# Optimization experiments

Measured on AMD Instinct MI355X. Metric: run time of the kernel, lower is better.

The kernel has to match this reference:

```python
import jax, jax.numpy as jnp
import numpy as np

LOW_THRESH = 0.3
HIGH_THRESH = 0.7
BATCH_SIZE = 256
NUM_POS = BATCH_SIZE // 2   # 128; guaranteed <= total_pos since B2=512 GT boxes are scattered positive
NUM_NEG = BATCH_SIZE - NUM_POS


def _xcycwh_to_x1y1x2y2(b):
    xc, yc, w, h = b[..., 0], b[..., 1], b[..., 2], b[..., 3]
    return jnp.stack([xc - w / 2, yc - h / 2, xc + w / 2, yc + h / 2], axis=-1)


def box_iou(box1, box2):
    # box1: (1, B1, 4), box2: (1, B2, 4) in (xc, yc, w, h) -> iou (1, B1, B2)
    area1 = box1[..., 2] * box1[..., 3]              # (1, B1)
    area2 = box2[..., 2] * box2[..., 3]              # (1, B2)
    c1 = _xcycwh_to_x1y1x2y2(box1)[:, :, None, :]    # (1, B1, 1, 4)
    c2 = _xcycwh_to_x1y1x2y2(box2)[:, None, :, :]    # (1, 1, B2, 4)
    x0 = jnp.maximum(c1[..., 0], c2[..., 0])
    y0 = jnp.maximum(c1[..., 1], c2[..., 1])
    x1 = jnp.minimum(c1[..., 2], c2[..., 2])
    y1 = jnp.minimum(c1[..., 3], c2[..., 3])
    inter = jnp.maximum(x1 - x0, 0.0) * jnp.maximum(y1 - y0, 0.0)  # (1, B1, B2)
    return inter / (area1[:, :, None] + area2[:, None, :] - inter)


def setup_inputs() -> dict:
    key = jax.random.key(0)
    k1, k2, k3, k4 = jax.random.split(key, 4)
    return {
        "input_boxes": jax.random.uniform(k1, (1, 50000, 4), dtype=jnp.float32),
        "target_boxes": jax.random.uniform(k2, (1, 512, 4), dtype=jnp.float32),
        "pos_noise": jax.random.uniform(k3, (50000,), dtype=jnp.float32),
        "neg_noise": jax.random.uniform(k4, (50000,), dtype=jnp.float32),
    }


def reference(input_boxes, target_boxes, pos_noise, neg_noise):
    ious = box_iou(input_boxes, target_boxes)        # (1, B1, B2)
    input_max_iou = jnp.max(ious, axis=2)            # (1, B1) best GT per proposal
    input_idx = jnp.argmax(ious, axis=2)             # (1, B1)
    target_idx = jnp.argmax(ious, axis=1)            # (1, B2) best proposal per GT

    pos_mask = input_max_iou[0] > HIGH_THRESH        # (B1,)
    neg_mask = input_max_iou[0] < LOW_THRESH
    # each GT's best-matching proposal is forced positive (scatter_)
    pos_mask = pos_mask.at[target_idx[0]].set(True)
    neg_mask = neg_mask.at[target_idx[0]].set(False)
    # fallback: if no negatives at all, negatives = complement of positives
    neg_mask = jnp.where(jnp.sum(neg_mask) == 0, ~pos_mask, neg_mask)

    # uniform sampling without replacement == top-k over iid uniform noise restricted to the mask
    pos_scores = jnp.where(pos_mask, pos_noise, -1.0)
    _, pos_input_idx = jax.lax.top_k(pos_scores, NUM_POS)      # (NUM_POS,)
    neg_scores = jnp.where(neg_mask, neg_noise, -1.0)
    _, neg_input_idx = jax.lax.top_k(neg_scores, NUM_NEG)      # (NUM_NEG,)

    pos_target_idx = input_idx[0][pos_input_idx]               # (NUM_POS,)
    return pos_input_idx, pos_target_idx, neg_input_idx
```

## Files before the change

kernel.cpp:

```cpp
#include <hip/hip_runtime.h>
#include <stdint.h>

#pragma clang fp contract(off)

typedef unsigned long long ull;

#define HIGHT 0.7f
#define LOWT  0.3f
#define KSEL  128
#define CAP   2048
#define MAXGT 512
#define TPB   256
#define CHUNK 32
#define TJ    128
#define SMP   132
#define NLAD  7

__device__ __constant__ float LADV[NLAD] = {0.998f, 0.99f, 0.95f, 0.8f, 0.5f, 0.25f, 0.0625f};

__device__ __forceinline__ float iou_pair(float ax0, float ay0, float ax1, float ay1, float aarea,
                                          float bx0, float by0, float bx1, float by1, float barea){
#pragma clang fp contract(off)
  float x0 = fmaxf(ax0, bx0);
  float y0 = fmaxf(ay0, by0);
  float x1 = fminf(ax1, bx1);
  float y1 = fminf(ay1, by1);
  float dx = fmaxf(x1 - x0, 0.0f);
  float dy = fmaxf(y1 - y0, 0.0f);
  float inter = dx * dy;
  float uni = (aarea + barea) - inter;
  return inter / uni;
}

__global__ __launch_bounds__(TPB)
void fused_iou(const float4* __restrict__ boxes, const float4* __restrict__ gts,
               int n1, int n2, int nblk,
               float* __restrict__ max_iou, int* __restrict__ input_idx,
               ull* __restrict__ colpart, int* __restrict__ forced,
               int* __restrict__ cnts_part, int* __restrict__ cnts,
               const float* __restrict__ pn, const float* __restrict__ nn)
{
#pragma clang fp contract(off)
  const int b = blockIdx.x, t = threadIdx.x;

  for (int x = b * TPB + t; x < n1; x += nblk * TPB) forced[x] = 0;
  if (b == 0 && t < 32) cnts[t] = 0;

  __shared__ float4 gc[MAXGT];
  __shared__ float  ga[MAXGT];
  __shared__ float  smat[CHUNK * SMP];
  __shared__ float  sm[CHUNK];

  for (int j = t; j < n2; j += TPB){
    float4 g = gts[j];
    float hw = g.z * 0.5f, hh = g.w * 0.5f;
    gc[j] = make_float4(g.x - hw, g.y - hh, g.x + hw, g.y + hh);
    ga[j] = g.z * g.w;
  }
  __syncthreads();

  const int lo = b * CHUNK;
  int cr = n1 - lo; if (cr > CHUNK) cr = CHUNK; if (cr < 0) cr = 0;

  const int pi = t >> 3, q = t & 7;
  const bool valid = (pi < cr);
  float px0 = 0, py0 = 0, px1 = 0, py1 = 0, pa = 0;
  if (valid){
    float4 pb = boxes[lo + pi];
    float hw = pb.z * 0.5f, hh = pb.w * 0.5f;
    px0 = pb.x - hw; py0 = pb.y - hh; px1 = pb.x + hw; py1 = pb.y + hh;
    pa = pb.z * pb.w;
  }
  float vA = -1.0f, vB = -1.0f, vC = -1.0f, vD = -1.0f;
  int jA = 0, jB = 0, jC = 0, jD = 0;

  for (int tb = 0; tb < n2; tb += TJ){
    const int tn = min(TJ, n2 - tb);
    if (valid){
      const int jlim = tb + tn;
      int j0 = tb + q;
      for (; j0 + 24 < jlim; j0 += 32){
        const int ja = j0, jb = j0 + 8, jc = j0 + 16, jd = j0 + 24;
        float4 gA = gc[ja]; float aA = ga[ja];
        float4 gB = gc[jb]; float aB = ga[jb];
        float4 gC = gc[jc]; float aC = ga[jc];
        float4 gD = gc[jd]; float aD = ga[jd];
        float u = iou_pair(px0, py0, px1, py1, pa, gA.x, gA.y, gA.z, gA.w, aA);
        float v = iou_pair(px0, py0, px1, py1, pa, gB.x, gB.y, gB.z, gB.w, aB);
        float w = iou_pair(px0, py0, px1, py1, pa, gC.x, gC.y, gC.z, gC.w, aC);
        float x = iou_pair(px0, py0, px1, py1, pa, gD.x, gD.y, gD.z, gD.w, aD);
        smat[pi * SMP + (ja - tb)] = u;
        smat[pi * SMP + (jb - tb)] = v;
        smat[pi * SMP + (jc - tb)] = w;
        smat[pi * SMP + (jd - tb)] = x;
        if (u > vA){ vA = u; jA = ja; }
        if (v > vB){ vB = v; jB = jb; }
        if (w > vC){ vC = w; jC = jc; }
        if (x > vD){ vD = x; jD = jd; }
      }
      for (; j0 < jlim; j0 += 8){
        float4 g0 = gc[j0]; float a0 = ga[j0];
        float u = iou_pair(px0, py0, px1, py1, pa, g0.x, g0.y, g0.z, g0.w, a0);
        smat[pi * SMP + (j0 - tb)] = u;
        if (u > vA){ vA = u; jA = j0; }
      }
    }
    __syncthreads();
    {
      const int jloc = t >> 1, half = t & 1;
      if (jloc < tn){
        float cv = -1.0f; int cp = 0;
        const int p0 = half * 16;
        const int p1 = min(p0 + 16, cr);
        for (int p = p0; p < p1; ++p){
          float v = smat[p * SMP + jloc];
          if (v > cv){ cv = v; cp = p; }
        }
        float ov = __shfl_xor(cv, 1, 64);
        int   op = __shfl_xor(cp, 1, 64);
        if (ov > cv || (ov == cv && op < cp)){ cv = ov; cp = op; }
        if (half == 0){
          colpart[(size_t)b * n2 + (tb + jloc)] =
            ((ull)__float_as_uint(cv) << 32) | (ull)(unsigned)~(unsigned)(lo + cp);
        }
      }
    }
    __syncthreads();
  }

  if (vB > vA || (vB == vA && jB < jA)){ vA = vB; jA = jB; }
  if (vC > vA || (vC == vA && jC < jA)){ vA = vC; jA = jC; }
  if (vD > vA || (vD == vA && jD < jA)){ vA = vD; jA = jD; }
  #pragma unroll
  for (int m = 1; m <= 4; m <<= 1){
    float ov = __shfl_xor(vA, m, 64);
    int   oj = __shfl_xor(jA, m, 64);
    if (ov > vA || (ov == vA && oj < jA)){ vA = ov; jA = oj; }
  }
  if (valid && q == 0){
    max_iou[lo + pi] = vA;
    input_idx[lo + pi] = jA;
    sm[pi] = vA;
  }
  __syncthreads();

  if (t < 64){
    const bool vld = (t < cr);
    float m = vld ? sm[t] : -1.0f;
    bool pos = vld && (m > HIGHT);
    bool nm  = vld && (m < LOWT);
    bool np  = vld && !(m > HIGHT);
    float sp = pos ? pn[lo + t] : -1.0f;
    float sn = (nm || np) ? nn[lo + t] : -1.0f;
    int c[24];
    c[0] = __popcll(__ballot(pos));
    c[1] = __popcll(__ballot(nm));
    c[2] = __popcll(__ballot(np));
    #pragma unroll
    for (int k = 0; k < NLAD; ++k){
      float L = LADV[k];
      c[3 + k]  = __popcll(__ballot(pos && sp > L));
      c[10 + k] = __popcll(__ballot(nm  && sn > L));
      c[17 + k] = __popcll(__ballot(np  && sn > L));
    }
    if (t == 0){
      #pragma unroll
      for (int k = 0; k < 24; ++k) cnts_part[b * 24 + k] = c[k];
    }
  }
}

__global__ __launch_bounds__(512)
void colfix3(const ull* __restrict__ colpart, int n1, int n2, int nblk,
             const float* __restrict__ max_iou,
             const float* __restrict__ pn, const float* __restrict__ nn,
             int* __restrict__ forced, const int* __restrict__ cnts_part,
             int* __restrict__ cnts)
{
  const int t = threadIdx.x, b = blockIdx.x, nb = gridDim.x;
  const int c = b * 8 + (t & 7);
  const int s = t >> 3;
  ull m = 0;
  if (c < n2){
    for (int r = s; r < nblk; r += 64){
      ull v = colpart[(size_t)r * n2 + c];
      if (v > m) m = v;
    }
  }
  __shared__ ull cm[8][64];
  cm[t & 7][s] = m;

  int csum = 0;
  if (t < 24){
    for (int x = b; x < nblk; x += nb) csum += cnts_part[x * 24 + t];
  }
  __syncthreads();
  if (t < 24 && csum) atomicAdd(&cnts[t], csum);

  if (t < 8){
    const int cc = b * 8 + t;
    if (cc < n2){
      ull best = 0;
      for (int k = 0; k < 64; ++k){ ull v = cm[t][k]; if (v > best) best = v; }
      unsigned idx = ~(unsigned)(best & 0xFFFFFFFFull);
      if (idx < (unsigned)n1){
        int old = atomicExch(&forced[idx], 1);
        if (old == 0){
          float m2 = max_iou[idx];
          if (!(m2 > HIGHT)){
            float sp = pn[idx];
            float sn = nn[idx];
            atomicAdd(&cnts[0], 1);
            atomicAdd(&cnts[2], -1);
            #pragma unroll
            for (int k = 0; k < NLAD; ++k){
              float L = LADV[k];
              if (sp > L) atomicAdd(&cnts[3 + k], 1);
              if (sn > L) atomicAdd(&cnts[17 + k], -1);
            }
            if (m2 < LOWT){
              atomicAdd(&cnts[1], -1);
              #pragma unroll
              for (int k = 0; k < NLAD; ++k)
                if (sn > LADV[k]) atomicAdd(&cnts[10 + k], -1);
            }
          }
        }
      }
    }
  }
}

__device__ __forceinline__ float pick_tau2(const int* lad){
  for (int k = 0; k < NLAD; ++k)
    if (lad[k] >= KSEL) return LADV[k];
  return -1.0f;
}

__global__ __launch_bounds__(1024)
void finalize(const float* __restrict__ max_iou, const int* __restrict__ forced,
              const float* __restrict__ pn, const float* __restrict__ nn,
              const int* __restrict__ cnts, const int* __restrict__ input_idx,
              int n1, int* __restrict__ out)
{
  const int t = threadIdx.x;
  const bool isPos = (blockIdx.x == 0);
  __shared__ int s_c[24];
  __shared__ int lcnt;
  __shared__ ull keys[CAP];
  if (t < 24) s_c[t] = cnts[t];
  if (t == 0) lcnt = 0;
  __syncthreads();
  const bool fb = (s_c[1] == 0);
  const int totM = isPos ? s_c[0] : (fb ? s_c[2] : s_c[1]);
  const float tau = isPos ? pick_tau2(&s_c[3]) : pick_tau2(fb ? &s_c[17] : &s_c[10]);
  const float* noise = isPos ? pn : nn;
  const bool fillOn = (totM < KSEL);

  const int n4 = n1 >> 2;
  for (int v = t; v < n4; v += 1024){
    const float4 m4 = reinterpret_cast<const float4*>(max_iou)[v];
    const int4  f4 = reinterpret_cast<const int4*>(forced)[v];
    const float4 s4 = reinterpret_cast<const float4*>(noise)[v];
    #pragma unroll
    for (int e = 0; e < 4; ++e){
      const float m  = (e==0)?m4.x:(e==1)?m4.y:(e==2)?m4.z:m4.w;
      const int   f  = (e==0)?f4.x:(e==1)?f4.y:(e==2)?f4.z:f4.w;
      const float sc = (e==0)?s4.x:(e==1)?s4.y:(e==2)?s4.z:s4.w;
      const int i = v * 4 + e;
      const bool pos = (m > HIGHT) || (f != 0);
      const bool sel = isPos ? pos : (fb ? (!pos) : ((m < LOWT) && f == 0));
      if (sel){
        if (sc > tau){
          int p = atomicAdd(&lcnt, 1);
          if (p < CAP) keys[p] = ((ull)(__float_as_uint(sc) + 1u) << 32) | (ull)(unsigned)~(unsigned)i;
        }
      } else if (fillOn && i < 2 * KSEL){
        int p = atomicAdd(&lcnt, 1);
        if (p < CAP) keys[p] = (ull)(unsigned)~(unsigned)i;
      }
    }
  }
  for (int i = (n4 << 2) + t; i < n1; i += 1024){
    const float m = max_iou[i];
    const int   f = forced[i];
    const float sc = noise[i];
    const bool pos = (m > HIGHT) || (f != 0);
    const bool sel = isPos ? pos : (fb ? (!pos) : ((m < LOWT) && f == 0));
    if (sel){
      if (sc > tau){
        int p = atomicAdd(&lcnt, 1);
        if (p < CAP) keys[p] = ((ull)(__float_as_uint(sc) + 1u) << 32) | (ull)(unsigned)~(unsigned)i;
      }
    } else if (fillOn && i < 2 * KSEL){
      int p = atomicAdd(&lcnt, 1);
      if (p < CAP) keys[p] = (ull)(unsigned)~(unsigned)i;
    }
  }
  __syncthreads();

  int n = lcnt; if (n > CAP) n = CAP;
  ull mk[2]; int mr[2];
  #pragma unroll
  for (int e = 0; e < 2; ++e){
    int x = t + e * 1024;
    mk[e] = (x < n) ? keys[x] : ~0ull;
    mr[e] = 0;
  }
  for (int o = 0; o < n; ++o){
    ull ko = keys[o];
    mr[0] += (ko > mk[0]);
    mr[1] += (ko > mk[1]);
  }
  #pragma unroll
  for (int e = 0; e < 2; ++e){
    int x = t + e * 1024;
    if (x < n && mr[e] < KSEL){
      unsigned idx = ~(unsigned)(mk[e] & 0xFFFFFFFFull);
      if (isPos){ out[mr[e]] = (int)idx; out[KSEL + mr[e]] = input_idx[idx]; }
      else        out[2 * KSEL + mr[e]] = (int)idx;
    }
  }
}

extern "C" void kernel_launch(void* const* d_in, const int* in_sizes, int n_in,
                              void* d_out, int out_size, void* d_ws, size_t ws_size,
                              hipStream_t stream){
  const float4* boxes = (const float4*)d_in[0];
  const float4* gts   = (const float4*)d_in[1];
  const float* pos_noise = (const float*)d_in[2];
  const float* neg_noise = (const float*)d_in[3];
  const int n1 = in_sizes[0] / 4;
  const int n2 = in_sizes[1] / 4;
  int* out = (int*)d_out;

  char* ws = (char*)d_ws;
  size_t off = 0;
  auto carve = [&](size_t bytes) -> char* {
    char* p = ws + off;
    off = (off + bytes + 255) & ~(size_t)255;
    return p;
  };
  const int nblk = (n1 + CHUNK - 1) / CHUNK;
  float* max_iou   = (float*)carve((size_t)n1 * 4);
  int*   input_idx = (int*)  carve((size_t)n1 * 4);
  ull*   colpart   = (ull*)  carve((size_t)nblk * n2 * 8);
  int*   forced    = (int*)  carve((size_t)n1 * 4);
  int*   cnts_part = (int*)  carve((size_t)nblk * 24 * 4);
  int*   cnts      = (int*)  carve(32 * 4);

  fused_iou<<<nblk, TPB, 0, stream>>>(boxes, gts, n1, n2, nblk,
                                      max_iou, input_idx, colpart, forced,
                                      cnts_part, cnts, pos_noise, neg_noise);
  const int cb = (n2 + 7) / 8;
  colfix3<<<cb, 512, 0, stream>>>(colpart, n1, n2, nblk, max_iou,
                                  pos_noise, neg_noise, forced, cnts_part, cnts);
  finalize<<<2, 1024, 0, stream>>>(max_iou, forced, pos_noise, neg_noise,
                                   cnts, input_idx, n1, out);
}
```

Before: 139.6 us.

## Replace global forced array with shared bitmap and row-parallel column reduction

```diff
diff --git a/kernel.cpp b/kernel.cpp
--- a/kernel.cpp
+++ b/kernel.cpp
@@ -11,10 +11,13 @@
 #define CAP   2048
 #define MAXGT 512
 #define TPB   256
+#define TPF   1024
 #define CHUNK 32
 #define TJ    128
 #define SMP   132
 #define NLAD  7
+#define NRB   96
+#define BMW   1568
 
 __device__ __constant__ float LADV[NLAD] = {0.998f, 0.99f, 0.95f, 0.8f, 0.5f, 0.25f, 0.0625f};
 
@@ -36,15 +39,18 @@
 void fused_iou(const float4* __restrict__ boxes, const float4* __restrict__ gts,
                int n1, int n2, int nblk,
                float* __restrict__ max_iou, int* __restrict__ input_idx,
-               ull* __restrict__ colpart, int* __restrict__ forced,
+               ull* __restrict__ colpart,
                int* __restrict__ cnts_part, int* __restrict__ cnts,
+               ull* __restrict__ colmax,
                const float* __restrict__ pn, const float* __restrict__ nn)
 {
 #pragma clang fp contract(off)
   const int b = blockIdx.x, t = threadIdx.x;
 
-  for (int x = b * TPB + t; x < n1; x += nblk * TPB) forced[x] = 0;
-  if (b == 0 && t < 32) cnts[t] = 0;
+  if (b == 0){
+    if (t < 32) cnts[t] = 0;
+    for (int x = t; x < n2; x += TPB) colmax[x] = 0;
+  }
 
   __shared__ float4 gc[MAXGT];
   __shared__ float  ga[MAXGT];
@@ -170,64 +176,28 @@
   }
 }
 
-__global__ __launch_bounds__(512)
-void colfix3(const ull* __restrict__ colpart, int n1, int n2, int nblk,
-             const float* __restrict__ max_iou,
-             const float* __restrict__ pn, const float* __restrict__ nn,
-             int* __restrict__ forced, const int* __restrict__ cnts_part,
-             int* __restrict__ cnts)
+__global__ __launch_bounds__(TPB)
+void colreduce2(const ull* __restrict__ colpart, int n2, int nblk,
+                const int* __restrict__ cnts_part,
+                int* __restrict__ cnts, ull* __restrict__ colmax)
 {
-  const int t = threadIdx.x, b = blockIdx.x, nb = gridDim.x;
-  const int c = b * 8 + (t & 7);
-  const int s = t >> 3;
-  ull m = 0;
-  if (c < n2){
-    for (int r = s; r < nblk; r += 64){
-      ull v = colpart[(size_t)r * n2 + c];
-      if (v > m) m = v;
-    }
-  }
-  __shared__ ull cm[8][64];
-  cm[t & 7][s] = m;
-
-  int csum = 0;
+  const int t = threadIdx.x, b = blockIdx.x;
+  ull m0 = 0, m1 = 0;
+  const int c0 = t, c1 = t + TPB;
+  for (int x = b; x < nblk; x += NRB){
+    const ull* row = colpart + (size_t)x * n2;
+    ull v0 = row[c0];
+    ull v1 = (c1 < n2) ? row[c1] : 0;
+    if (v0 > m0) m0 = v0;
+    if (v1 > m1) m1 = v1;
+  }
+  if (c0 < n2 && m0) atomicMax(&colmax[c0], m0);
+  if (c1 < n2 && m1) atomicMax(&colmax[c1], m1);
+
   if (t < 24){
-    for (int x = b; x < nblk; x += nb) csum += cnts_part[x * 24 + t];
-  }
-  __syncthreads();
-  if (t < 24 && csum) atomicAdd(&cnts[t], csum);
-
-  if (t < 8){
-    const int cc = b * 8 + t;
-    if (cc < n2){
-      ull best = 0;
-      for (int k = 0; k < 64; ++k){ ull v = cm[t][k]; if (v > best) best = v; }
-      unsigned idx = ~(unsigned)(best & 0xFFFFFFFFull);
-      if (idx < (unsigned)n1){
-        int old = atomicExch(&forced[idx], 1);
-        if (old == 0){
-          float m2 = max_iou[idx];
-          if (!(m2 > HIGHT)){
-            float sp = pn[idx];
-            float sn = nn[idx];
-            atomicAdd(&cnts[0], 1);
-            atomicAdd(&cnts[2], -1);
-            #pragma unroll
-            for (int k = 0; k < NLAD; ++k){
-              float L = LADV[k];
-              if (sp > L) atomicAdd(&cnts[3 + k], 1);
-              if (sn > L) atomicAdd(&cnts[17 + k], -1);
-            }
-            if (m2 < LOWT){
-              atomicAdd(&cnts[1], -1);
-              #pragma unroll
-              for (int k = 0; k < NLAD; ++k)
-                if (sn > LADV[k]) atomicAdd(&cnts[10 + k], -1);
-            }
-          }
-        }
-      }
-    }
+    int s = 0;
+    for (int x = b; x < nblk; x += NRB) s += cnts_part[x * 24 + t];
+    if (s) atomicAdd(&cnts[t], s);
   }
 }
 
@@ -237,20 +207,54 @@
   return -1.0f;
 }
 
-__global__ __launch_bounds__(1024)
-void finalize(const float* __restrict__ max_iou, const int* __restrict__ forced,
-              const float* __restrict__ pn, const float* __restrict__ nn,
-              const int* __restrict__ cnts, const int* __restrict__ input_idx,
-              int n1, int* __restrict__ out)
+__global__ __launch_bounds__(TPF)
+void finalize2(const ull* __restrict__ colmax, int n1, int n2,
+               const float* __restrict__ max_iou, const int* __restrict__ input_idx,
+               const float* __restrict__ pn, const float* __restrict__ nn,
+               const int* __restrict__ cnts, int* __restrict__ out)
 {
   const int t = threadIdx.x;
   const bool isPos = (blockIdx.x == 0);
   __shared__ int s_c[24];
+  __shared__ int bm[BMW];
   __shared__ int lcnt;
   __shared__ ull keys[CAP];
+
   if (t < 24) s_c[t] = cnts[t];
   if (t == 0) lcnt = 0;
-  __syncthreads();
+  for (int x = t; x < BMW; x += TPF) bm[x] = 0;
+  __syncthreads();
+
+  if (t < n2){
+    ull key = colmax[t];
+    unsigned idx = ~(unsigned)(key & 0xFFFFFFFFull);
+    if (idx < (unsigned)n1){
+      int old = atomicOr(&bm[idx >> 5], 1 << (idx & 31));
+      if (!(old & (1 << (idx & 31)))){
+        float m2 = max_iou[idx];
+        if (!(m2 > HIGHT)){
+          float sp = pn[idx];
+          float sn = nn[idx];
+          atomicAdd(&s_c[0], 1);
+          atomicAdd(&s_c[2], -1);
+          #pragma unroll
+          for (int k = 0; k < NLAD; ++k){
+            float L = LADV[k];
+            if (sp > L) atomicAdd(&s_c[3 + k], 1);
+            if (sn > L) atomicAdd(&s_c[17 + k], -1);
+          }
+          if (m2 < LOWT){
+            atomicAdd(&s_c[1], -1);
+            #pragma unroll
+            for (int k = 0; k < NLAD; ++k)
+              if (sn > LADV[k]) atomicAdd(&s_c[10 + k], -1);
+          }
+        }
+      }
+    }
+  }
+  __syncthreads();
+
   const bool fb = (s_c[1] == 0);
   const int totM = isPos ? s_c[0] : (fb ? s_c[2] : s_c[1]);
   const float tau = isPos ? pick_tau2(&s_c[3]) : pick_tau2(fb ? &s_c[17] : &s_c[10]);
@@ -258,18 +262,17 @@
   const bool fillOn = (totM < KSEL);
 
   const int n4 = n1 >> 2;
-  for (int v = t; v < n4; v += 1024){
+  for (int v = t; v < n4; v += TPF){
     const float4 m4 = reinterpret_cast<const float4*>(max_iou)[v];
-    const int4  f4 = reinterpret_cast<const int4*>(forced)[v];
     const float4 s4 = reinterpret_cast<const float4*>(noise)[v];
     #pragma unroll
     for (int e = 0; e < 4; ++e){
       const float m  = (e==0)?m4.x:(e==1)?m4.y:(e==2)?m4.z:m4.w;
-      const int   f  = (e==0)?f4.x:(e==1)?f4.y:(e==2)?f4.z:f4.w;
       const float sc = (e==0)?s4.x:(e==1)?s4.y:(e==2)?s4.z:s4.w;
       const int i = v * 4 + e;
-      const bool pos = (m > HIGHT) || (f != 0);
-      const bool sel = isPos ? pos : (fb ? (!pos) : ((m < LOWT) && f == 0));
+      const bool f = (bm[i >> 5] >> (i & 31)) & 1;
+      const bool pos = (m > HIGHT) || f;
+      const bool sel = isPos ? pos : (fb ? (!pos) : ((m < LOWT) && !f));
       if (sel){
         if (sc > tau){
           int p = atomicAdd(&lcnt, 1);
@@ -281,12 +284,12 @@
       }
     }
   }
-  for (int i = (n4 << 2) + t; i < n1; i += 1024){
+  for (int i = (n4 << 2) + t; i < n1; i += TPF){
     const float m = max_iou[i];
-    const int   f = forced[i];
     const float sc = noise[i];
-    const bool pos = (m > HIGHT) || (f != 0);
-    const bool sel = isPos ? pos : (fb ? (!pos) : ((m < LOWT) && f == 0));
+    const bool f = (bm[i >> 5] >> (i & 31)) & 1;
+    const bool pos = (m > HIGHT) || f;
+    const bool sel = isPos ? pos : (fb ? (!pos) : ((m < LOWT) && !f));
     if (sel){
       if (sc > tau){
         int p = atomicAdd(&lcnt, 1);
@@ -303,7 +306,7 @@
   ull mk[2]; int mr[2];
   #pragma unroll
   for (int e = 0; e < 2; ++e){
-    int x = t + e * 1024;
+    int x = t + e * TPF;
     mk[e] = (x < n) ? keys[x] : ~0ull;
     mr[e] = 0;
   }
@@ -314,7 +317,7 @@
   }
   #pragma unroll
   for (int e = 0; e < 2; ++e){
-    int x = t + e * 1024;
+    int x = t + e * TPF;
     if (x < n && mr[e] < KSEL){
       unsigned idx = ~(unsigned)(mk[e] & 0xFFFFFFFFull);
       if (isPos){ out[mr[e]] = (int)idx; out[KSEL + mr[e]] = input_idx[idx]; }
@@ -345,16 +348,14 @@
   float* max_iou   = (float*)carve((size_t)n1 * 4);
   int*   input_idx = (int*)  carve((size_t)n1 * 4);
   ull*   colpart   = (ull*)  carve((size_t)nblk * n2 * 8);
-  int*   forced    = (int*)  carve((size_t)n1 * 4);
   int*   cnts_part = (int*)  carve((size_t)nblk * 24 * 4);
   int*   cnts      = (int*)  carve(32 * 4);
+  ull*   colmax    = (ull*)  carve((size_t)MAXGT * 8);
 
   fused_iou<<<nblk, TPB, 0, stream>>>(boxes, gts, n1, n2, nblk,
-                                      max_iou, input_idx, colpart, forced,
-                                      cnts_part, cnts, pos_noise, neg_noise);
-  const int cb = (n2 + 7) / 8;
-  colfix3<<<cb, 512, 0, stream>>>(colpart, n1, n2, nblk, max_iou,
-                                  pos_noise, neg_noise, forced, cnts_part, cnts);
-  finalize<<<2, 1024, 0, stream>>>(max_iou, forced, pos_noise, neg_noise,
-                                   cnts, input_idx, n1, out);
-}
+                                      max_iou, input_idx, colpart,
+                                      cnts_part, cnts, colmax, pos_noise, neg_noise);
+  colreduce2<<<NRB, TPB, 0, stream>>>(colpart, n2, nblk, cnts_part, cnts, colmax);
+  finalize2<<<2, TPF, 0, stream>>>(colmax, n1, n2, max_iou, input_idx,
+                                   pos_noise, neg_noise, cnts, out);
+}
```

After: 135.0 us. -3.3%, faster.
